# Optimization experiments

Measured on AMD Instinct MI355X. Metric: run time of the kernel, lower is better.

## Reference

```python
import jax, jax.numpy as jnp
import numpy as np

N_PER = 20000   # nodes per node-type
NDIM = 3        # number of node types / feature lists
N = N_PER * NDIM
H = 256         # n_hidden
R = 5           # e_type (num relations)
C = 16          # n_class
E = 600000      # num edges
L = 2           # n_layers
LEA = 0.3       # LeakyReLU slope


def setup_inputs() -> dict:
    key = jax.random.key(0)
    ks = iter(jax.random.split(key, 64))
    def w(shape, s=0.05):
        return jax.random.normal(next(ks), shape, jnp.float32) * s
    inp = {}
    inp['feat0'] = jax.random.normal(next(ks), (N_PER, 100), jnp.float32)
    inp['feat1'] = jax.random.normal(next(ks), (N_PER, 300), jnp.float32)
    inp['feat2'] = jax.random.normal(next(ks), (N_PER, 768), jnp.float32)
    inp['src'] = jax.random.randint(next(ks), (E,), 0, N, jnp.int32)
    inp['dst'] = jax.random.randint(next(ks), (E,), 0, N, jnp.int32)
    inp['etypes'] = jax.random.randint(next(ks), (E,), 0, R, jnp.int32)
    # encoder 0: in_feat=100 <= 128 -> Linear(100,H), LReLU, Linear(H,H)
    inp['e0w1'] = w((100, H)); inp['e0b1'] = w((H,))
    inp['e0w2'] = w((H, H));   inp['e0b2'] = w((H,))
    # encoder 1: in_feat=300 <= 512 -> Linear(300,256), LReLU, Linear(256,H)
    inp['e1w1'] = w((300, 256)); inp['e1b1'] = w((256,))
    inp['e1w2'] = w((256, H));   inp['e1b2'] = w((H,))
    # encoder 2: in_feat=768 <= 1024 -> Linear(768,512), LReLU, Linear(512,256), LReLU, Linear(256,H)
    inp['e2w1'] = w((768, 512)); inp['e2b1'] = w((512,))
    inp['e2w2'] = w((512, 256)); inp['e2b2'] = w((256,))
    inp['e2w3'] = w((256, H));   inp['e2b3'] = w((H,))
    # RelGraphConv layers: per-relation weight, self-loop weight, bias
    inp['gW'] = w((L, R, H, H)); inp['gL'] = w((L, H, H)); inp['gB'] = w((L, H))
    # decoder: Linear(H,256), LReLU, Linear(256,C)
    inp['dw1'] = w((H, 256)); inp['db1'] = w((256,))
    inp['dw2'] = w((256, C)); inp['db2'] = w((C,))
    # constr_encoder: Linear(C,1024), LReLU, Linear(1024,H)
    inp['cew1'] = w((C, 1024)); inp['ceb1'] = w((1024,))
    inp['cew2'] = w((1024, H)); inp['ceb2'] = w((H,))
    # constr_decoder: Linear(H,256), LReLU, Linear(256,C)
    inp['cdw1'] = w((H, 256)); inp['cdb1'] = w((256,))
    inp['cdw2'] = w((256, C)); inp['cdb2'] = w((C,))
    return inp


def _lrelu(x):
    return jnp.where(x > 0, x, LEA * x)


def reference(feat0, feat1, feat2, e0w1, e0b1, e0w2, e0b2, e1w1, e1b1, e1w2, e1b2,
              e2w1, e2b1, e2w2, e2b2, e2w3, e2b3, gW, gL, gB,
              dw1, db1, dw2, db2, cew1, ceb1, cew2, ceb2, cdw1, cdb1, cdw2, cdb2,
              src, dst, etypes):
    # per-type encoders (dropout = identity at inference)
    h0 = _lrelu(feat0 @ e0w1 + e0b1) @ e0w2 + e0b2
    h1 = _lrelu(feat1 @ e1w1 + e1b1) @ e1w2 + e1b2
    h2 = _lrelu(_lrelu(feat2 @ e2w1 + e2b1) @ e2w2 + e2b2) @ e2w3 + e2b3
    h = jnp.concatenate([h0, h1, h2], axis=0)  # [N, H]
    n_nodes = h.shape[0]
    src64 = src.astype(jnp.int32)
    # RelGraphConv layers: m_e = W_{r(e)} h_src; h' = sum_in(m) + h @ W_loop + b
    for l in range(L):
        proj = jnp.einsum('nh,rhg->rng', h, gW[l])        # [R, N, H]
        msgs = proj[etypes, src64]                         # [E, H] relation-indexed gather
        agg = jax.ops.segment_sum(msgs, dst, num_segments=n_nodes)
        h = agg + h @ gL[l] + gB[l]
    feat = _lrelu(h @ dw1 + db1) @ dw2 + db2               # [N, C] decoder
    cf = _lrelu(feat @ cew1 + ceb1) @ cew2 + ceb2          # constr_encoder
    cf = _lrelu(cf @ cdw1 + cdb1) @ cdw2 + cdb2            # constr_decoder -> [N, C]
    con_loss = jnp.mean((cf - feat) ** 2)                  # reconstruction constraint loss
    # triple-nested loop == segment mean over the NDIM node-type blocks
    res = cf.reshape(NDIM, n_nodes // NDIM, C).mean(axis=0)  # [N/NDIM, C]
    return res, con_loss
```

## Files before the change

### kernel.cpp

```cpp
#include <hip/hip_runtime.h>
#include <stdint.h>

#define E_NUM 600000
#define N_NODES 60000
#define NPER 20000
#define NKEY 300000
#define MROW 60032
#define HPAD 60160
#define MP20 20096
#define KA 1536

typedef __attribute__((ext_vector_type(8))) short frag8;
typedef __attribute__((ext_vector_type(4))) float facc4;

__device__ __forceinline__ float bf2f(uint16_t u) {
  union { uint32_t i; float f; } v; v.i = ((uint32_t)u) << 16; return v.f;
}
__device__ __forceinline__ uint16_t f2bf(float f) {
  union { float f; uint32_t i; } v; v.f = f;
  uint32_t r = v.i + 0x7FFFu + ((v.i >> 16) & 1u);
  return (uint16_t)(r >> 16);
}
__device__ __forceinline__ uint16_t in2bf(const void* p, size_t i, int mode) {
  return mode ? f2bf(((const float*)p)[i]) : ((const uint16_t*)p)[i];
}

template<int ACT>
__global__ __launch_bounds__(256)
void gemm_bt(const uint16_t* __restrict__ A, int lda,
             const uint16_t* __restrict__ Bt, int ldb,
             const uint16_t* __restrict__ bias, uint16_t* __restrict__ C,
             int N, int K)
{
  __shared__ __align__(16) uint16_t sA[128 * 32];
  __shared__ __align__(16) uint16_t sB[128 * 32];
  const int tid = threadIdx.x;
  const int lane = tid & 63;
  const size_t mbase = (size_t)blockIdx.x * 128;
  const size_t nbase = (size_t)blockIdx.y * 128;
  const int wave = tid >> 6;
  const int wm = (wave >> 1) * 64;
  const int wn = (wave & 1) * 64;

  const uint16_t* Ab = A + mbase * lda;
  const uint16_t* Bb = Bt + nbase * ldb;

  facc4 acc[4][4] = {};

  const int nk = K >> 5;
  for (int kt = 0; kt < nk; ++kt) {
    const int kb = kt << 5;
#pragma unroll
    for (int it = 0; it < 2; ++it) {
      const int c = it * 256 + tid;
      const int r = c >> 2;
      const int kc = (c & 3) * 8;
      uint4 va = *(const uint4*)(Ab + (size_t)r * lda + kb + kc);
      uint4 vb = *(const uint4*)(Bb + (size_t)r * ldb + kb + kc);
      *(uint4*)(sA + (size_t)c * 8) = va;
      *(uint4*)(sB + (size_t)c * 8) = vb;
    }
    __syncthreads();
    {
      const int m15 = lane & 15, q8 = (lane >> 4) * 8;
      frag8 af[4], bfr[4];
#pragma unroll
      for (int i = 0; i < 4; ++i)
        af[i] = *(const frag8*)(sA + (size_t)(wm + i * 16 + m15) * 32 + q8);
#pragma unroll
      for (int j = 0; j < 4; ++j)
        bfr[j] = *(const frag8*)(sB + (size_t)(wn + j * 16 + m15) * 32 + q8);
#pragma unroll
      for (int i = 0; i < 4; ++i)
#pragma unroll
        for (int j = 0; j < 4; ++j)
          acc[i][j] = __builtin_amdgcn_mfma_f32_16x16x32_bf16(af[i], bfr[j], acc[i][j], 0, 0, 0);
    }
    __syncthreads();
  }

  const int m15 = lane & 15;
  const int r4 = (lane >> 4) * 4;
#pragma unroll
  for (int j = 0; j < 4; ++j) {
    const size_t col = nbase + wn + j * 16 + m15;
    const float bv = bias ? bf2f(bias[col]) : 0.f;
#pragma unroll
    for (int i = 0; i < 4; ++i) {
      const size_t row0 = mbase + wm + i * 16 + r4;
#pragma unroll
      for (int r = 0; r < 4; ++r) {
        float v = acc[i][j][r] + bv;
        if (ACT) v = v > 0.f ? v : 0.3f * v;
        C[(row0 + r) * (size_t)N + col] = f2bf(v);
      }
    }
  }
}

template<int MODE>
__global__ __launch_bounds__(256)
void gemv16_k(const uint16_t* __restrict__ A, const uint16_t* __restrict__ W,
              const uint16_t* __restrict__ bias, float* __restrict__ outf,
              uint16_t* __restrict__ padout)
{
  __shared__ float sW[256 * 16];
  for (int i = threadIdx.x; i < 4096; i += 256) sW[i] = bf2f(W[i]);
  __syncthreads();
  const int row = blockIdx.x * 16 + (threadIdx.x >> 4);
  const int col = threadIdx.x & 15;
  const uint16_t* ar = A + (size_t)row * 256;
  float acc = 0.f;
#pragma unroll
  for (int k = 0; k < 256; k += 8) {
    uint4 w4 = *(const uint4*)(ar + k);
    const uint16_t* pw = (const uint16_t*)&w4;
#pragma unroll
    for (int j = 0; j < 8; ++j) acc += bf2f(pw[j]) * sW[(k + j) * 16 + col];
  }
  acc += bf2f(bias[col]);
  outf[(size_t)row * 16 + col] = acc;
  if (MODE == 0) {
    padout[(size_t)row * 32 + col] = f2bf(acc);
    padout[(size_t)row * 32 + 16 + col] = 0;
  }
}

__global__ void probe_k(const uint16_t* __restrict__ f0, int* __restrict__ mode) {
  long i = (long)blockIdx.x * 256 + threadIdx.x;
  int bad = 0;
  for (; i < 2000000; i += (long)gridDim.x * 256)
    bad |= (((f0[i] >> 7) & 0xFFu) == 0xFFu);
  if (bad) atomicOr(mode, 1);
}

struct TDesc { const void* src; uint16_t* dst; long soff; int K, N, Kp, dstLd, dstOff; };
struct TPack { TDesc d[23]; int n; };

__global__ void transpose_k(TPack p, const int* __restrict__ modep) {
  const TDesc t = p.d[blockIdx.y];
  const int mode = *modep;
  const int total = t.N * t.Kp;
  for (int i = blockIdx.x * 256 + threadIdx.x; i < total; i += gridDim.x * 256) {
    const int n = i / t.Kp, k = i - n * t.Kp;
    t.dst[(size_t)n * t.dstLd + t.dstOff + k] =
        (k < t.K) ? in2bf(t.src, (size_t)(t.soff + (long)k * t.N + n), mode)
                  : (uint16_t)0;
  }
}

struct BDesc { const void* src; int n; int dstoff; };
struct BPack { BDesc d[16]; int n; };

__global__ void biasconv_k(BPack p, uint16_t* __restrict__ arena,
                           const int* __restrict__ modep) {
  const BDesc b = p.d[blockIdx.y];
  const int mode = *modep;
  for (int i = blockIdx.x * 256 + threadIdx.x; i < b.n; i += gridDim.x * 256)
    arena[b.dstoff + i] = in2bf(b.src, i, mode);
}

__global__ void repack_k(const void* __restrict__ in, uint16_t* __restrict__ out,
                         int row0, int Mvalid, int Kin, int Kpad, int rowsOut,
                         const int* __restrict__ modep)
{
  const int mode = *modep;
  const int total = rowsOut * Kpad;
  for (int i = blockIdx.x * 256 + threadIdx.x; i < total; i += gridDim.x * 256) {
    const int m = i / Kpad, k = i - m * Kpad;
    const int sm = row0 + m;
    out[i] = (sm < Mvalid && k < Kin) ? in2bf(in, (size_t)sm * Kin + k, mode)
                                      : (uint16_t)0;
  }
}

__global__ void zfill_k(uint16_t* p, int n) {
  int i = blockIdx.x * 256 + threadIdx.x;
  if (i < n) p[i] = 0;
}

__global__ void init_k(int* deg5, int* mode, float* lossAcc) {
  int i = blockIdx.x * 256 + threadIdx.x;
  if (i < NKEY) deg5[i] = 0;
  if (i == NKEY) { *mode = 0; *lossAcc = 0.f; }
}

__global__ void hist5_k(const int* __restrict__ dst, const int* __restrict__ ety,
                        int* __restrict__ deg5) {
  int e = blockIdx.x * 256 + threadIdx.x;
  if (e < E_NUM) atomicAdd(&deg5[dst[e] * 5 + ety[e]], 1);
}

__global__ __launch_bounds__(1024) void scan1_k(const int* __restrict__ deg,
                                                int* __restrict__ offs, int* __restrict__ bsum) {
  __shared__ int s[1024];
  const int i = blockIdx.x * 1024 + threadIdx.x;
  int v = (i < NKEY) ? deg[i] : 0;
  s[threadIdx.x] = v; __syncthreads();
  for (int d = 1; d < 1024; d <<= 1) {
    int x = (threadIdx.x >= d) ? s[threadIdx.x - d] : 0;
    __syncthreads();
    s[threadIdx.x] += x; __syncthreads();
  }
  if (i < NKEY) offs[i + 1] = s[threadIdx.x];
  if (threadIdx.x == 1023) bsum[blockIdx.x] = s[1023];
}

__global__ void scan2_k(int* bsum) {
  if (threadIdx.x == 0 && blockIdx.x == 0) {
    int run = 0;
    for (int b = 0; b < 293; ++b) { int t = bsum[b]; bsum[b] = run; run += t; }
  }
}

__global__ __launch_bounds__(1024) void scan3_k(const int* __restrict__ deg,
                                                int* __restrict__ offs, int* __restrict__ cursor,
                                                const int* __restrict__ bsum) {
  const int i = blockIdx.x * 1024 + threadIdx.x;
  if (i >= NKEY) return;
  const int t = offs[i + 1] + bsum[blockIdx.x];
  offs[i + 1] = t;
  cursor[i] = t - deg[i];
  if (i == 0) offs[0] = 0;
}

__global__ void scatter5_k(const int* __restrict__ src, const int* __restrict__ dst,
                           const int* __restrict__ ety, int* __restrict__ cursor,
                           int* __restrict__ payload) {
  int e = blockIdx.x * 256 + threadIdx.x;
  if (e >= E_NUM) return;
  int key = dst[e] * 5 + ety[e];
  int pos = atomicAdd(&cursor[key], 1);
  payload[pos] = src[e];
}

__global__ __launch_bounds__(256)
void gather_all_k(const uint16_t* __restrict__ h, const int* __restrict__ offs5,
                  const int* __restrict__ payload, uint16_t* __restrict__ Abuf)
{
  const int node = blockIdx.x * 4 + (threadIdx.x >> 6);
  const int lane = threadIdx.x & 63;
  uint16_t* arow = Abuf + (size_t)node * KA + lane * 4;
  if (node >= N_NODES) {
#pragma unroll
    for (int b = 0; b < 6; ++b) *(uint64_t*)(arow + b * 256) = 0;
    return;
  }
  *(uint64_t*)arow = *(const uint64_t*)(h + (size_t)node * 256 + lane * 4);
  const int base = node * 5;
#pragma unroll
  for (int r = 0; r < 5; ++r) {
    const int o0 = offs5[base + r], o1 = offs5[base + r + 1];
    float a0 = 0.f, a1 = 0.f, a2 = 0.f, a3 = 0.f;
    for (int e = o0; e < o1; ++e) {
      const int s = payload[e];
      uint64_t w = *(const uint64_t*)(h + (size_t)s * 256 + lane * 4);
      a0 += bf2f((uint16_t)w);         a1 += bf2f((uint16_t)(w >> 16));
      a2 += bf2f((uint16_t)(w >> 32)); a3 += bf2f((uint16_t)(w >> 48));
    }
    uint64_t o = (uint64_t)f2bf(a0) | ((uint64_t)f2bf(a1) << 16)
               | ((uint64_t)f2bf(a2) << 32) | ((uint64_t)f2bf(a3) << 48);
    *(uint64_t*)(arow + (1 + r) * 256) = o;
  }
}

__global__ void sentinel_k(uint16_t* out, float code) {
  int i = blockIdx.x * 256 + threadIdx.x;
  if (i > 320000) return;
  out[i] = (i == 0) ? f2bf(code) : (uint16_t)0;
}

__global__ __launch_bounds__(256) void loss_k(const float* __restrict__ cf,
                                              const float* __restrict__ feat,
                                              float* __restrict__ acc) {
  __shared__ float s[256];
  float p = 0.f;
  for (int i = blockIdx.x * 256 + threadIdx.x; i < N_NODES * 16; i += gridDim.x * 256) {
    float d = cf[i] - feat[i];
    p += d * d;
  }
  s[threadIdx.x] = p; __syncthreads();
  for (int d = 128; d > 0; d >>= 1) {
    if (threadIdx.x < d) s[threadIdx.x] += s[threadIdx.x + d];
    __syncthreads();
  }
  if (threadIdx.x == 0) atomicAdd(acc, s[0]);
}

__global__ void final_k(const float* __restrict__ cf, const float* __restrict__ lossAcc,
                        const int* __restrict__ modep, void* __restrict__ outv)
{
  int i = blockIdx.x * 256 + threadIdx.x;
  if (i > 320000) return;
  float v = (i == 320000) ? *lossAcc * (1.f / 960000.f)
                          : (cf[i] + cf[i + 320000] + cf[i + 640000]) * (1.f / 3.f);
  if (*modep) ((float*)outv)[i] = v;
  else ((uint16_t*)outv)[i] = f2bf(v);
}

extern "C" void kernel_launch(void* const* d_in, const int* in_sizes, int n_in,
                              void* d_out, int out_size, void* d_ws, size_t ws_size,
                              hipStream_t stream)
{
  (void)in_sizes; (void)n_in; (void)out_size;
  const void* feat0 = d_in[0];
  const void* feat1 = d_in[1];
  const void* feat2 = d_in[2];
  const int* srcI = (const int*)d_in[3];
  const int* dstI = (const int*)d_in[4];
  const int* etyI = (const int*)d_in[5];
  const void *e0w1 = d_in[6],  *e0b1 = d_in[7],  *e0w2 = d_in[8],  *e0b2 = d_in[9];
  const void *e1w1 = d_in[10], *e1b1 = d_in[11], *e1w2 = d_in[12], *e1b2 = d_in[13];
  const void *e2w1 = d_in[14], *e2b1 = d_in[15], *e2w2 = d_in[16], *e2b2 = d_in[17];
  const void *e2w3 = d_in[18], *e2b3 = d_in[19];
  const void *gW = d_in[20], *gL = d_in[21], *gB = d_in[22];
  const void *dw1 = d_in[23], *db1 = d_in[24], *dw2 = d_in[25], *db2 = d_in[26];
  const void *cew1 = d_in[27], *ceb1 = d_in[28], *cew2 = d_in[29], *ceb2 = d_in[30];
  const void *cdw1 = d_in[31], *cdb1 = d_in[32], *cdw2 = d_in[33], *cdb2 = d_in[34];

  uint8_t* base = (uint8_t*)d_ws;
  size_t off = 0;
  auto alloc = [&](size_t bytes) -> void* {
    void* p = base + off;
    off += (bytes + 255) & ~(size_t)255;
    return p;
  };
  int* modep    = (int*)alloc(4);
  int* bsum     = (int*)alloc(512 * 4);
  float* lossAcc = (float*)alloc(4);
  int* deg5    = (int*)alloc((size_t)NKEY * 4);
  int* offs5   = (int*)alloc((size_t)(NKEY + 33) * 4);
  int* cursor5 = (int*)alloc((size_t)NKEY * 4);
  int* payload = (int*)alloc((size_t)E_NUM * 4);
  auto wal = [&](size_t elems) { return (uint16_t*)alloc(elems * 2); };
  uint16_t* arena = wal(12576);
  uint16_t* e0w1t = wal(256 * 128);
  uint16_t* e0w2t = wal(256 * 256);
  uint16_t* e1w1t = wal(256 * 320);
  uint16_t* e1w2t = wal(256 * 256);
  uint16_t* e2w1t = wal(512 * 768);
  uint16_t* e2w2t = wal(256 * 512);
  uint16_t* e2w3t = wal(256 * 256);
  uint16_t* dw1t  = wal(256 * 256);
  uint16_t* cew1t = wal(1024 * 32);
  uint16_t* cew2t = wal(256 * 1024);
  uint16_t* cdw1t = wal(256 * 256);
  uint16_t* wall0 = wal(256 * KA);
  uint16_t* wall1 = wal(256 * KA);
  uint16_t* h1 = wal((size_t)HPAD * 256);
  uint16_t* h2 = wal((size_t)HPAD * 256);
  uint16_t* Abuf = wal((size_t)HPAD * KA);

  if (off > ws_size) {
    float wsmb = (float)(ws_size >> 20);
    if (wsmb > 512.f) wsmb = 512.f;
    sentinel_k<<<dim3(1251), 256, 0, stream>>>((uint16_t*)d_out, 10000.f + 16.f * wsmb);
    return;
  }

  enum { oE0B1 = 0, oE0B2 = 256, oE1B1 = 512, oE1B2 = 768, oE2B1 = 1024,
         oE2B2 = 1536, oE2B3 = 1792, oGB = 2048, oDB1 = 2560, oDB2 = 2816,
         oCEB1 = 2832, oCEB2 = 3856, oCDB1 = 4112, oCDB2 = 4368,
         oDW2 = 4384, oCDW2 = 8480 };

  uint16_t* f0p   = Abuf;
  uint16_t* eTmp0 = Abuf + 2572288;
  uint16_t* f1p   = Abuf;
  uint16_t* eTmp1 = Abuf + 6430720;
  uint16_t* f2p   = Abuf;
  uint16_t* tEnc  = Abuf + 15433728;
  uint16_t* eEnc  = Abuf + 25722880;
  uint16_t* Hc      = Abuf;
  uint16_t* featpad = Abuf + 61472768;
  float*    featf   = (float*)(Abuf + 63393792);
  float*    cff     = (float*)(Abuf + 67233792);

  init_k<<<dim3(1173), 256, 0, stream>>>(deg5, modep, lossAcc);
  probe_k<<<dim3(512), 256, 0, stream>>>((const uint16_t*)feat0, modep);
  hist5_k<<<dim3(2344), 256, 0, stream>>>(dstI, etyI, deg5);
  scan1_k<<<dim3(293), 1024, 0, stream>>>(deg5, offs5, bsum);
  scan2_k<<<dim3(1), 64, 0, stream>>>(bsum);
  scan3_k<<<dim3(293), 1024, 0, stream>>>(deg5, offs5, cursor5, bsum);
  scatter5_k<<<dim3(2344), 256, 0, stream>>>(srcI, dstI, etyI, cursor5, payload);

  BPack bp; int nb = 0;
  auto addB = [&](const void* s, int n, int dstoff) {
    bp.d[nb].src = s; bp.d[nb].n = n; bp.d[nb].dstoff = dstoff; ++nb;
  };
  addB(e0b1, 256, oE0B1); addB(e0b2, 256, oE0B2);
  addB(e1b1, 256, oE1B1); addB(e1b2, 256, oE1B2);
  addB(e2b1, 512, oE2B1); addB(e2b2, 256, oE2B2); addB(e2b3, 256, oE2B3);
  addB(gB, 512, oGB);
  addB(db1, 256, oDB1); addB(db2, 16, oDB2);
  addB(ceb1, 1024, oCEB1); addB(ceb2, 256, oCEB2);
  addB(cdb1, 256, oCDB1); addB(cdb2, 16, oCDB2);
  addB(dw2, 4096, oDW2); addB(cdw2, 4096, oCDW2);
  bp.n = nb;
  biasconv_k<<<dim3(16, nb), 256, 0, stream>>>(bp, arena, modep);

  TPack tp; int nd = 0;
  auto addT = [&](const void* s, long soff, uint16_t* d, int K, int N, int Kp,
                  int dstLd, int dstOff) {
    tp.d[nd].src = s; tp.d[nd].soff = soff; tp.d[nd].dst = d;
    tp.d[nd].K = K; tp.d[nd].N = N; tp.d[nd].Kp = Kp;
    tp.d[nd].dstLd = dstLd; tp.d[nd].dstOff = dstOff; ++nd;
  };
  addT(e0w1, 0, e0w1t, 100, 256, 128, 128, 0);
  addT(e0w2, 0, e0w2t, 256, 256, 256, 256, 0);
  addT(e1w1, 0, e1w1t, 300, 256, 320, 320, 0);
  addT(e1w2, 0, e1w2t, 256, 256, 256, 256, 0);
  addT(e2w1, 0, e2w1t, 768, 512, 768, 768, 0);
  addT(e2w2, 0, e2w2t, 512, 256, 512, 512, 0);
  addT(e2w3, 0, e2w3t, 256, 256, 256, 256, 0);
  addT(dw1,  0, dw1t,  256, 256, 256, 256, 0);
  addT(cew1, 0, cew1t, 16, 1024, 32, 32, 0);
  addT(cew2, 0, cew2t, 1024, 256, 1024, 1024, 0);
  addT(cdw1, 0, cdw1t, 256, 256, 256, 256, 0);
  uint16_t* walls[2] = { wall0, wall1 };
  for (int l = 0; l < 2; ++l) {
    addT(gL, (long)l * 65536, walls[l], 256, 256, 256, KA, 0);
    for (int r = 0; r < 5; ++r)
      addT(gW, (long)(l * 5 + r) * 65536, walls[l], 256, 256, 256, KA, 256 + r * 256);
  }
  tp.n = nd;
  transpose_k<<<dim3(48, nd), 256, 0, stream>>>(tp, modep);

  repack_k<<<dim3(2048), 256, 0, stream>>>(feat0, f0p, 0, NPER, 100, 128, MP20, modep);
  gemm_bt<1><<<dim3(157, 2), 256, 0, stream>>>(f0p, 128, e0w1t, 128, arena + oE0B1, eTmp0, 256, 128);
  gemm_bt<0><<<dim3(157, 2), 256, 0, stream>>>(eTmp0, 256, e0w2t, 256, arena + oE0B2, h1, 256, 256);
  repack_k<<<dim3(2048), 256, 0, stream>>>(feat1, f1p, 0, NPER, 300, 320, MP20, modep);
  gemm_bt<1><<<dim3(157, 2), 256, 0, stream>>>(f1p, 320, e1w1t, 320, arena + oE1B1, eTmp1, 256, 320);
  gemm_bt<0><<<dim3(157, 2), 256, 0, stream>>>(eTmp1, 256, e1w2t, 256, arena + oE1B2, h1 + (size_t)NPER * 256, 256, 256);
  repack_k<<<dim3(4096), 256, 0, stream>>>(feat2, f2p, 0, NPER, 768, 768, MP20, modep);
  gemm_bt<1><<<dim3(157, 4), 256, 0, stream>>>(f2p, 768, e2w1t, 768, arena + oE2B1, tEnc, 512, 768);
  gemm_bt<1><<<dim3(157, 2), 256, 0, stream>>>(tEnc, 512, e2w2t, 512, arena + oE2B2, eEnc, 256, 512);
  gemm_bt<0><<<dim3(157, 2), 256, 0, stream>>>(eEnc, 256, e2w3t, 256, arena + oE2B3,
                                               h1 + (size_t)2 * NPER * 256, 256, 256);

  uint16_t* hbuf[2] = { h1, h2 };
  for (int l = 0; l < 2; ++l) {
    uint16_t* hin  = hbuf[l & 1];
    uint16_t* hout = hbuf[(l + 1) & 1];
    gather_all_k<<<dim3(15040), 256, 0, stream>>>(hin, offs5, payload, Abuf);
    gemm_bt<0><<<dim3(469, 2), 256, 0, stream>>>(Abuf, KA, walls[l], KA,
                                                 arena + oGB + l * 256, hout, 256, KA);
  }

  gemm_bt<1><<<dim3(469, 2), 256, 0, stream>>>(h1, 256, dw1t, 256, arena + oDB1, h2, 256, 256);
  gemv16_k<0><<<dim3(3750), 256, 0, stream>>>(h2, arena + oDW2, arena + oDB2, featf, featpad);
  zfill_k<<<dim3(4), 256, 0, stream>>>(featpad + (size_t)N_NODES * 32, 32 * 32);

  gemm_bt<1><<<dim3(469, 8), 256, 0, stream>>>(featpad, 32, cew1t, 32, arena + oCEB1, Hc, 1024, 32);
  gemm_bt<0><<<dim3(469, 2), 256, 0, stream>>>(Hc, 1024, cew2t, 1024, arena + oCEB2, h1, 256, 1024);

  gemm_bt<1><<<dim3(469, 2), 256, 0, stream>>>(h1, 256, cdw1t, 256, arena + oCDB1, h2, 256, 256);
  gemv16_k<1><<<dim3(3750), 256, 0, stream>>>(h2, arena + oCDW2, arena + oCDB2, cff, nullptr);

  loss_k<<<dim3(512), 256, 0, stream>>>(cff, featf, lossAcc);
  final_k<<<dim3(1251), 256, 0, stream>>>(cff, lossAcc, modep, d_out);
}
```

Before: 1.052 ms.

## Use direct global-to-LDS loads with XOR swizzle in GEMM and vectorize input repack

The GEMM tile loads now use the global_load_lds builtin to copy 16-byte chunks straight into shared memory, skipping the register round trip. They also apply an XOR swizzle on the k-chunk index to reduce LDS bank conflicts when reading MFMA fragments. Feature repacking now converts four elements per thread with vector loads and stores, and the gather kernel skips zero-filling rows beyond the padded height. The direct-to-LDS path depends on the wave-contiguous destination layout matching the swizzled read pattern, and repack4 assumes row lengths (100, 300, 768) are multiples of four so vector loads stay in bounds.

```diff
diff --git a/kernel.cpp b/kernel.cpp
--- a/kernel.cpp
+++ b/kernel.cpp
@@ -23,6 +23,12 @@
 }
 __device__ __forceinline__ uint16_t in2bf(const void* p, size_t i, int mode) {
   return mode ? f2bf(((const float*)p)[i]) : ((const uint16_t*)p)[i];
+}
+
+typedef __attribute__((address_space(3))) uint32_t lds_u32;
+typedef const __attribute__((address_space(1))) uint32_t glb_u32;
+__device__ __forceinline__ void gl_lds16(const uint16_t* g, uint16_t* l) {
+  __builtin_amdgcn_global_load_lds((glb_u32*)g, (lds_u32*)l, 16, 0, 0);
 }
 
 template<int ACT>
@@ -54,22 +60,25 @@
     for (int it = 0; it < 2; ++it) {
       const int c = it * 256 + tid;
       const int r = c >> 2;
-      const int kc = (c & 3) * 8;
-      uint4 va = *(const uint4*)(Ab + (size_t)r * lda + kb + kc);
-      uint4 vb = *(const uint4*)(Bb + (size_t)r * ldb + kb + kc);
-      *(uint4*)(sA + (size_t)c * 8) = va;
-      *(uint4*)(sB + (size_t)c * 8) = vb;
+      const int kc = ((c & 3) ^ (r & 3)) * 8;
+      gl_lds16(Ab + (size_t)r * lda + kb + kc, sA + (size_t)(it * 256 + wave * 64) * 8);
+      gl_lds16(Bb + (size_t)r * ldb + kb + kc, sB + (size_t)(it * 256 + wave * 64) * 8);
     }
     __syncthreads();
     {
-      const int m15 = lane & 15, q8 = (lane >> 4) * 8;
+      const int m15 = lane & 15;
+      const int q = lane >> 4;
       frag8 af[4], bfr[4];
 #pragma unroll
-      for (int i = 0; i < 4; ++i)
-        af[i] = *(const frag8*)(sA + (size_t)(wm + i * 16 + m15) * 32 + q8);
-#pragma unroll
-      for (int j = 0; j < 4; ++j)
-        bfr[j] = *(const frag8*)(sB + (size_t)(wn + j * 16 + m15) * 32 + q8);
+      for (int i = 0; i < 4; ++i) {
+        const int row = wm + i * 16 + m15;
+        af[i] = *(const frag8*)(sA + (size_t)row * 32 + (q ^ (row & 3)) * 8);
+      }
+#pragma unroll
+      for (int j = 0; j < 4; ++j) {
+        const int row = wn + j * 16 + m15;
+        bfr[j] = *(const frag8*)(sB + (size_t)row * 32 + (q ^ (row & 3)) * 8);
+      }
 #pragma unroll
       for (int i = 0; i < 4; ++i)
 #pragma unroll
@@ -160,17 +169,29 @@
     arena[b.dstoff + i] = in2bf(b.src, i, mode);
 }
 
-__global__ void repack_k(const void* __restrict__ in, uint16_t* __restrict__ out,
-                         int row0, int Mvalid, int Kin, int Kpad, int rowsOut,
-                         const int* __restrict__ modep)
+__global__ void repack4_k(const void* __restrict__ in, uint16_t* __restrict__ out,
+                          int row0, int Mvalid, int Kin, int Kpad, int rowsOut,
+                          const int* __restrict__ modep)
 {
   const int mode = *modep;
-  const int total = rowsOut * Kpad;
-  for (int i = blockIdx.x * 256 + threadIdx.x; i < total; i += gridDim.x * 256) {
-    const int m = i / Kpad, k = i - m * Kpad;
+  const int kq4 = Kpad >> 2;
+  const int total = rowsOut * kq4;
+  for (int idx = blockIdx.x * 256 + threadIdx.x; idx < total; idx += gridDim.x * 256) {
+    const int m = idx / kq4;
+    const int k = (idx - m * kq4) * 4;
     const int sm = row0 + m;
-    out[i] = (sm < Mvalid && k < Kin) ? in2bf(in, (size_t)sm * Kin + k, mode)
-                                      : (uint16_t)0;
+    uint64_t pack = 0;
+    if (sm < Mvalid && k < Kin) {
+      const size_t s = (size_t)sm * Kin + k;
+      if (mode) {
+        float4 f = *(const float4*)((const float*)in + s);
+        pack = (uint64_t)f2bf(f.x) | ((uint64_t)f2bf(f.y) << 16)
+             | ((uint64_t)f2bf(f.z) << 32) | ((uint64_t)f2bf(f.w) << 48);
+      } else {
+        pack = *(const uint64_t*)((const uint16_t*)in + s);
+      }
+    }
+    *(uint64_t*)(out + (size_t)m * Kpad + k) = pack;
   }
 }
 
@@ -242,8 +263,10 @@
   const int lane = threadIdx.x & 63;
   uint16_t* arow = Abuf + (size_t)node * KA + lane * 4;
   if (node >= N_NODES) {
-#pragma unroll
-    for (int b = 0; b < 6; ++b) *(uint64_t*)(arow + b * 256) = 0;
+    if (node < HPAD) {
+#pragma unroll
+      for (int b = 0; b < 6; ++b) *(uint64_t*)(arow + b * 256) = 0;
+    }
     return;
   }
   *(uint64_t*)arow = *(const uint64_t*)(h + (size_t)node * 256 + lane * 4);
@@ -254,9 +277,9 @@
     float a0 = 0.f, a1 = 0.f, a2 = 0.f, a3 = 0.f;
     for (int e = o0; e < o1; ++e) {
       const int s = payload[e];
-      uint64_t w = *(const uint64_t*)(h + (size_t)s * 256 + lane * 4);
-      a0 += bf2f((uint16_t)w);         a1 += bf2f((uint16_t)(w >> 16));
-      a2 += bf2f((uint16_t)(w >> 32)); a3 += bf2f((uint16_t)(w >> 48));
+      uint64_t v = *(const uint64_t*)(h + (size_t)s * 256 + lane * 4);
+      a0 += bf2f((uint16_t)v);         a1 += bf2f((uint16_t)(v >> 16));
+      a2 += bf2f((uint16_t)(v >> 32)); a3 += bf2f((uint16_t)(v >> 48));
     }
     uint64_t o = (uint64_t)f2bf(a0) | ((uint64_t)f2bf(a1) << 16)
                | ((uint64_t)f2bf(a2) << 32) | ((uint64_t)f2bf(a3) << 48);
@@ -425,13 +448,13 @@
   tp.n = nd;
   transpose_k<<<dim3(48, nd), 256, 0, stream>>>(tp, modep);
 
-  repack_k<<<dim3(2048), 256, 0, stream>>>(feat0, f0p, 0, NPER, 100, 128, MP20, modep);
+  repack4_k<<<dim3(1024), 256, 0, stream>>>(feat0, f0p, 0, NPER, 100, 128, MP20, modep);
   gemm_bt<1><<<dim3(157, 2), 256, 0, stream>>>(f0p, 128, e0w1t, 128, arena + oE0B1, eTmp0, 256, 128);
   gemm_bt<0><<<dim3(157, 2), 256, 0, stream>>>(eTmp0, 256, e0w2t, 256, arena + oE0B2, h1, 256, 256);
-  repack_k<<<dim3(2048), 256, 0, stream>>>(feat1, f1p, 0, NPER, 300, 320, MP20, modep);
+  repack4_k<<<dim3(1024), 256, 0, stream>>>(feat1, f1p, 0, NPER, 300, 320, MP20, modep);
   gemm_bt<1><<<dim3(157, 2), 256, 0, stream>>>(f1p, 320, e1w1t, 320, arena + oE1B1, eTmp1, 256, 320);
   gemm_bt<0><<<dim3(157, 2), 256, 0, stream>>>(eTmp1, 256, e1w2t, 256, arena + oE1B2, h1 + (size_t)NPER * 256, 256, 256);
-  repack_k<<<dim3(4096), 256, 0, stream>>>(feat2, f2p, 0, NPER, 768, 768, MP20, modep);
+  repack4_k<<<dim3(2048), 256, 0, stream>>>(feat2, f2p, 0, NPER, 768, 768, MP20, modep);
   gemm_bt<1><<<dim3(157, 4), 256, 0, stream>>>(f2p, 768, e2w1t, 768, arena + oE2B1, tEnc, 512, 768);
   gemm_bt<1><<<dim3(157, 2), 256, 0, stream>>>(tEnc, 512, e2w2t, 512, arena + oE2B2, eEnc, 256, 512);
   gemm_bt<0><<<dim3(157, 2), 256, 0, stream>>>(eEnc, 256, e2w3t, 256, arena + oE2B3,
```

Result: faster. 1.024 ms (-2.6%).
